# Kernel optimization log

Measured on AMD Instinct MI355X. Metric: run time of the kernel, lower is better.

Reference implementation:

```python
import jax, jax.numpy as jnp
import numpy as np

N = 50000      # input_dim == output_dim
E = 800000     # nnz in sparse weight (original: 12300 from w_ind.mat)
B = 64         # batch


def setup_inputs() -> dict:
    key = jax.random.key(0)
    k1, k2, k3, k4, k5 = jax.random.split(key, 5)
    inputs = jax.random.normal(k1, (B, N), dtype=jnp.float32)
    # truncated-normal(std=0.01) approximated by scaled normal
    W3 = 0.01 * jax.random.normal(k2, (E,), dtype=jnp.float32)
    b = jnp.zeros((N,), dtype=jnp.float32)
    # velocity = 1250 * row of CSV -> positive scale vector
    velocity = 1250.0 * jax.random.uniform(k3, (N,), dtype=jnp.float32)
    I = jax.random.randint(k4, (E,), 0, N, dtype=jnp.int64)  # row (dest) index
    J = jax.random.randint(k5, (E,), 0, N, dtype=jnp.int64)  # col (source) index
    return {"inputs": inputs, "W3": W3, "b": b, "velocity": velocity, "I": I, "J": J}


def reference(inputs, W3, b, velocity, I, J):
    # sparse W[i,j] = W3[e] scaled by velocity broadcast along rows -> * velocity[J]
    wv = W3 * velocity[J]                       # [E]
    # out = (W_sparse @ inputs^T)^T + b  == scatter-add over rows I
    contrib = inputs[:, J] * wv[None, :]        # [B, E] gather + scale
    out = jnp.zeros((inputs.shape[0], velocity.shape[0]), inputs.dtype)
    out = out.at[:, I].add(contrib)             # [B, N] scatter-add
    return out + b
```

## Files before the change

kernel.cpp:

```cpp
#include <hip/hip_runtime.h>


#define BATCH 64
#define QROWS 64
#define PCHUNK 2048
#define GCH 512
#define BCAP 32
#define BSTR 33
#define GSTR 16

typedef unsigned long long ull;

__global__ void __launch_bounds__(256) k_prep_hist(
        const float* __restrict__ in, const float* __restrict__ velocity,
        float* __restrict__ in_T,
        const int* __restrict__ I, int* __restrict__ coarse_hist,
        int NC, int N, int E, int nb_n) {
    __shared__ float tile[64 * 65];
    const int t = threadIdx.x;

    if ((int)blockIdx.x < nb_n) {
        const int n0 = blockIdx.x * 64;
        const int x  = t & 63;
        const int r  = t >> 6;
        for (int b = r; b < BATCH; b += 4) {
            float v = 0.f;
            if (n0 + x < N) v = in[(size_t)b * N + n0 + x];
            tile[x * 65 + b] = v;
        }
        __syncthreads();
        for (int xr = r; xr < 64; xr += 4) {
            if (n0 + xr < N) {
                const float vel = velocity[n0 + xr];
                in_T[(size_t)(n0 + xr) * BATCH + x] = tile[xr * 65 + x] * vel;
            }
        }
    } else {
        int* h = (int*)tile;
        for (int c = t; c < NC; c += 256) h[c] = 0;
        __syncthreads();
        const int e0 = ((int)blockIdx.x - nb_n) * PCHUNK;
        int e1 = e0 + PCHUNK; if (e1 > E) e1 = E;
        for (int e = e0 + t; e < e1; e += 256) atomicAdd(&h[I[e] >> 6], 1);
        __syncthreads();
        for (int c = t; c < NC; c += 256) if (h[c]) atomicAdd(&coarse_hist[c], h[c]);
    }
}

__global__ void __launch_bounds__(1024) k_scan(const int* __restrict__ coarse_hist,
                                               int* __restrict__ coarse_base,
                                               int* __restrict__ gcursor, int NC) {
    __shared__ int sh[1024];
    const int t = threadIdx.x;
    const int v = (t < NC) ? coarse_hist[t] : 0;
    sh[t] = v;
    __syncthreads();
    for (int off = 1; off < 1024; off <<= 1) {
        const int u = (t >= off) ? sh[t - off] : 0;
        __syncthreads();
        sh[t] += u;
        __syncthreads();
    }
    if (t < NC) { coarse_base[t] = sh[t] - v; gcursor[t * GSTR] = sh[t] - v; }
    if (t == NC - 1) coarse_base[NC] = sh[t];
}

__global__ void __launch_bounds__(512) k_partition(
        const int* __restrict__ I, const int* __restrict__ J,
        const float* __restrict__ W3,
        int* __restrict__ gcursor, ull* __restrict__ part, int E, int NC) {
    __shared__ int hist[1024];
    __shared__ int base[1024];
    const int t = threadIdx.x;
    for (int c = t; c < NC; c += 512) hist[c] = 0;
    __syncthreads();
    const int e0 = blockIdx.x * PCHUNK;
    int e1 = e0 + PCHUNK; if (e1 > E) e1 = E;

    ull  rec[4];
    int  cb[4];
    int  rk[4];
    bool ok[4];
    #pragma unroll
    for (int u = 0; u < 4; ++u) {
        const int e = e0 + u * 512 + t;
        ok[u] = (e < e1);
        cb[u] = 0; rk[u] = 0; rec[u] = 0ull;
        if (ok[u]) {
            const int i = I[e];
            const int j = J[e];
            cb[u] = i >> 6;
            rk[u] = atomicAdd(&hist[cb[u]], 1);
            rec[u] = ((ull)__float_as_uint(W3[e]) << 32)
                   | ((ull)((unsigned)(i & 63) << 16) | (unsigned)j);
        }
    }
    __syncthreads();
    for (int c = t; c < NC; c += 512) {
        const int cnt = hist[c];
        base[c] = cnt ? atomicAdd(&gcursor[c * GSTR], cnt) : 0;
    }
    __syncthreads();
    #pragma unroll
    for (int u = 0; u < 4; ++u)
        if (ok[u]) part[(size_t)base[cb[u]] + rk[u]] = rec[u];
}

__global__ void __launch_bounds__(512) k_gather(
        const float* __restrict__ in_T, const ull* __restrict__ part,
        const int* __restrict__ coarse_base, const float* __restrict__ bias,
        float* __restrict__ out, int N) {
    __shared__ ull smem[64 * BSTR + GCH];
    __shared__ int cnt[64];
    __shared__ int ocnt;
    ull* const bins = smem;
    ull* const ovf  = smem + 64 * BSTR;
    float* const tile = (float*)smem;

    const int t    = threadIdx.x;
    const int lane = t & 63;
    const int w    = t >> 6;
    const int c    = blockIdx.x;

    const int beg = coarse_base[c];
    const int end = coarse_base[c + 1];

    float acc[8];
    #pragma unroll
    for (int r = 0; r < 8; ++r) acc[r] = 0.f;

    for (int cb = beg; cb < end; cb += GCH) {
        __syncthreads();
        if (t < 64) cnt[t] = 0;
        if (t == 0) ocnt = 0;
        __syncthreads();

        const int e = cb + t;
        if (e < end) {
            const ull rec = part[e];
            const int li = (int)(((unsigned)rec >> 16) & 63u);
            const int r = atomicAdd(&cnt[li], 1);
            if (r < BCAP) bins[li * BSTR + r] = rec;
            else          ovf[atomicAdd(&ocnt, 1)] = rec;
        }
        __syncthreads();

        #pragma unroll
        for (int r8 = 0; r8 < 8; ++r8) {
            const int row = w * 8 + r8;
            int n = cnt[row]; if (n > BCAP) n = BCAP;
            const ull* bp = &bins[row * BSTR];
            float a = acc[r8];
            int k = 0;
            for (; k + 4 <= n; k += 4) {
                const ull r0 = bp[k], r1 = bp[k + 1], r2 = bp[k + 2], r3 = bp[k + 3];
                const float v0 = in_T[(int)((unsigned)r0 & 0xffffu) * BATCH + lane];
                const float v1 = in_T[(int)((unsigned)r1 & 0xffffu) * BATCH + lane];
                const float v2 = in_T[(int)((unsigned)r2 & 0xffffu) * BATCH + lane];
                const float v3 = in_T[(int)((unsigned)r3 & 0xffffu) * BATCH + lane];
                a += v0 * __uint_as_float((unsigned)(r0 >> 32));
                a += v1 * __uint_as_float((unsigned)(r1 >> 32));
                a += v2 * __uint_as_float((unsigned)(r2 >> 32));
                a += v3 * __uint_as_float((unsigned)(r3 >> 32));
            }
            for (; k < n; ++k) {
                const ull rr = bp[k];
                a += in_T[(int)((unsigned)rr & 0xffffu) * BATCH + lane]
                   * __uint_as_float((unsigned)(rr >> 32));
            }
            acc[r8] = a;
        }

        const int oc = ocnt;
        if (oc > 0) {
            #pragma unroll
            for (int r8 = 0; r8 < 8; ++r8) {
                const int row = w * 8 + r8;
                float a = acc[r8];
                for (int k = 0; k < oc; ++k) {
                    const ull rr = ovf[k];
                    if ((int)(((unsigned)rr >> 16) & 63u) == row)
                        a += in_T[(int)((unsigned)rr & 0xffffu) * BATCH + lane]
                           * __uint_as_float((unsigned)(rr >> 32));
                }
                acc[r8] = a;
            }
        }
    }

    __syncthreads();
    #pragma unroll
    for (int r8 = 0; r8 < 8; ++r8)
        tile[(w * 8 + r8) * 65 + lane] = acc[r8];
    __syncthreads();

    const int n0  = c * QROWS;
    const int row = t & 63;
    const int bq  = t >> 6;
    const int n = n0 + row;
    if (n < N) {
        const float bv = bias[n];
        for (int b = bq; b < BATCH; b += 8)
            out[(size_t)b * N + n] = tile[row * 65 + b] + bv;
    }
}

__global__ void k_edge_scatter_direct(const float* __restrict__ in,
                                      const float* __restrict__ W3,
                                      const float* __restrict__ velocity,
                                      const int* __restrict__ I,
                                      const int* __restrict__ J,
                                      float* __restrict__ out, int N, int E) {
    const int lane = threadIdx.x & 63;
    const long wave   = (long)blockIdx.x * (blockDim.x >> 6) + (threadIdx.x >> 6);
    const long nwaves = (long)gridDim.x * (blockDim.x >> 6);
    for (long base = wave * 64; base < E; base += nwaves * 64) {
        const long e = base + lane;
        int iv = 0, jv = 0; float wvv = 0.f;
        if (e < E) { iv = I[e]; jv = J[e]; wvv = W3[e] * velocity[jv]; }
        const int cnt = (int)((E - base) < 64 ? (E - base) : 64);
        for (int k = 0; k < cnt; ++k) {
            const int   ii = __shfl(iv, k);
            const int   jj = __shfl(jv, k);
            const float wvx = __shfl(wvv, k);
            const float val = in[(size_t)lane * N + jj] * wvx;
            atomicAdd(&out[(size_t)lane * N + ii], val);
        }
    }
}

__global__ void k_add_bias(const float* __restrict__ bias, float* __restrict__ out, int N, int total) {
    int idx = blockIdx.x * blockDim.x + threadIdx.x;
    if (idx < total) out[idx] += bias[idx % N];
}

extern "C" void kernel_launch(void* const* d_in, const int* in_sizes, int n_in,
                              void* d_out, int out_size, void* d_ws, size_t ws_size,
                              hipStream_t stream) {
    const float* inputs   = (const float*)d_in[0];
    const float* W3       = (const float*)d_in[1];
    const float* bias     = (const float*)d_in[2];
    const float* velocity = (const float*)d_in[3];
    const int*   I        = (const int*)d_in[4];
    const int*   J        = (const int*)d_in[5];
    const int E = in_sizes[1];
    const int N = in_sizes[3];
    float* out = (float*)d_out;

    const size_t mat_elems = (size_t)N * BATCH;
    const int NC   = (N + QROWS - 1) / QROWS;
    const int nb_n = (N + 63) / 64;
    const int nb_e = (E + PCHUNK - 1) / PCHUNK;

    const size_t need = mat_elems * sizeof(float)
                      + (size_t)E * sizeof(ull)
                      + (size_t)(NC + (NC + 1) + NC * GSTR) * sizeof(int);

    if (ws_size >= need && N <= 65535 && NC <= 1024) {
        float* in_T        = (float*)d_ws;
        ull*   part        = (ull*)(in_T + mat_elems);
        int*   coarse_hist = (int*)(part + E);
        int*   coarse_base = coarse_hist + NC;
        int*   gcursor     = coarse_base + NC + 1;

        hipMemsetAsync(coarse_hist, 0, (size_t)NC * sizeof(int), stream);
        k_prep_hist<<<nb_n + nb_e, 256,  0, stream>>>(inputs, velocity, in_T, I, coarse_hist, NC, N, E, nb_n);
        k_scan     <<<1,           1024, 0, stream>>>(coarse_hist, coarse_base, gcursor, NC);
        k_partition<<<nb_e,        512,  0, stream>>>(I, J, W3, gcursor, part, E, NC);
        k_gather   <<<NC,          512,  0, stream>>>(in_T, part, coarse_base, bias, out, N);
    } else {
        hipMemsetAsync(out, 0, (size_t)out_size * sizeof(float), stream);
        const int waves_needed   = (E + 63) / 64;
        const int scatter_blocks = (waves_needed + 3) / 4;
        k_edge_scatter_direct<<<scatter_blocks, 256, 0, stream>>>(inputs, W3, velocity, I, J, out, N, E);
        k_add_bias<<<(out_size + 255) / 256, 256, 0, stream>>>(bias, out, N, out_size);
    }
}
```

Measured before the change: 156.5 us.

## Fuse scan into prep kernel via last-block pattern and enlarge gather chunk

```diff
diff --git a/kernel.cpp b/kernel.cpp
--- a/kernel.cpp
+++ b/kernel.cpp
@@ -4,7 +4,7 @@
 #define BATCH 64
 #define QROWS 64
 #define PCHUNK 2048
-#define GCH 512
+#define GCH 1024
 #define BCAP 32
 #define BSTR 33
 #define GSTR 16
@@ -15,8 +15,12 @@
         const float* __restrict__ in, const float* __restrict__ velocity,
         float* __restrict__ in_T,
         const int* __restrict__ I, int* __restrict__ coarse_hist,
-        int NC, int N, int E, int nb_n) {
+        int* __restrict__ done, int* __restrict__ coarse_base,
+        int* __restrict__ gcursor,
+        int NC, int N, int E, int nb_n, int ntotal) {
     __shared__ float tile[64 * 65];
+    __shared__ int ps[256];
+    __shared__ int amlast;
     const int t = threadIdx.x;
 
     if ((int)blockIdx.x < nb_n) {
@@ -45,24 +49,42 @@
         __syncthreads();
         for (int c = t; c < NC; c += 256) if (h[c]) atomicAdd(&coarse_hist[c], h[c]);
     }
-}
-
-__global__ void __launch_bounds__(1024) k_scan(const int* __restrict__ coarse_hist,
-                                               int* __restrict__ coarse_base,
-                                               int* __restrict__ gcursor, int NC) {
-    __shared__ int sh[1024];
-    const int t = threadIdx.x;
-    const int v = (t < NC) ? coarse_hist[t] : 0;
-    sh[t] = v;
-    __syncthreads();
-    for (int off = 1; off < 1024; off <<= 1) {
-        const int u = (t >= off) ? sh[t - off] : 0;
-        __syncthreads();
-        sh[t] += u;
-        __syncthreads();
-    }
-    if (t < NC) { coarse_base[t] = sh[t] - v; gcursor[t * GSTR] = sh[t] - v; }
-    if (t == NC - 1) coarse_base[NC] = sh[t];
+
+    __syncthreads();
+    if (t == 0) {
+        __threadfence();
+        amlast = (atomicAdd(done, 1) == ntotal - 1) ? 1 : 0;
+    }
+    __syncthreads();
+    if (amlast) {
+        int loc[4];
+        int s = 0;
+        #pragma unroll
+        for (int k = 0; k < 4; ++k) {
+            const int c = 4 * t + k;
+            int v = 0;
+            if (c < NC) v = atomicAdd(&coarse_hist[c], 0);
+            loc[k] = s; s += v;
+        }
+        ps[t] = s;
+        __syncthreads();
+        for (int off = 1; off < 256; off <<= 1) {
+            const int u = (t >= off) ? ps[t - off] : 0;
+            __syncthreads();
+            ps[t] += u;
+            __syncthreads();
+        }
+        const int excl = ps[t] - s;
+        #pragma unroll
+        for (int k = 0; k < 4; ++k) {
+            const int c = 4 * t + k;
+            if (c < NC) {
+                coarse_base[c]    = excl + loc[k];
+                gcursor[c * GSTR] = excl + loc[k];
+            }
+        }
+        if (t == 255) coarse_base[NC] = ps[255];
+    }
 }
 
 __global__ void __launch_bounds__(512) k_partition(
@@ -135,13 +157,16 @@
         if (t == 0) ocnt = 0;
         __syncthreads();
 
-        const int e = cb + t;
-        if (e < end) {
-            const ull rec = part[e];
-            const int li = (int)(((unsigned)rec >> 16) & 63u);
-            const int r = atomicAdd(&cnt[li], 1);
-            if (r < BCAP) bins[li * BSTR + r] = rec;
-            else          ovf[atomicAdd(&ocnt, 1)] = rec;
+        #pragma unroll
+        for (int u = 0; u < 2; ++u) {
+            const int e = cb + u * 512 + t;
+            if (e < end) {
+                const ull rec = part[e];
+                const int li = (int)(((unsigned)rec >> 16) & 63u);
+                const int r = atomicAdd(&cnt[li], 1);
+                if (r < BCAP) bins[li * BSTR + r] = rec;
+                else          ovf[atomicAdd(&ocnt, 1)] = rec;
+            }
         }
         __syncthreads();
 
@@ -251,23 +276,26 @@
     const int NC   = (N + QROWS - 1) / QROWS;
     const int nb_n = (N + 63) / 64;
     const int nb_e = (E + PCHUNK - 1) / PCHUNK;
+    const int ntot = nb_n + nb_e;
 
     const size_t need = mat_elems * sizeof(float)
                       + (size_t)E * sizeof(ull)
-                      + (size_t)(NC + (NC + 1) + NC * GSTR) * sizeof(int);
+                      + (size_t)(NC + 1 + (NC + 1) + NC * GSTR) * sizeof(int);
 
     if (ws_size >= need && N <= 65535 && NC <= 1024) {
         float* in_T        = (float*)d_ws;
         ull*   part        = (ull*)(in_T + mat_elems);
         int*   coarse_hist = (int*)(part + E);
-        int*   coarse_base = coarse_hist + NC;
+        int*   done        = coarse_hist + NC;
+        int*   coarse_base = done + 1;
         int*   gcursor     = coarse_base + NC + 1;
 
-        hipMemsetAsync(coarse_hist, 0, (size_t)NC * sizeof(int), stream);
-        k_prep_hist<<<nb_n + nb_e, 256,  0, stream>>>(inputs, velocity, in_T, I, coarse_hist, NC, N, E, nb_n);
-        k_scan     <<<1,           1024, 0, stream>>>(coarse_hist, coarse_base, gcursor, NC);
-        k_partition<<<nb_e,        512,  0, stream>>>(I, J, W3, gcursor, part, E, NC);
-        k_gather   <<<NC,          512,  0, stream>>>(in_T, part, coarse_base, bias, out, N);
+        hipMemsetAsync(coarse_hist, 0, (size_t)(NC + 1) * sizeof(int), stream);
+        k_prep_hist<<<ntot, 256,  0, stream>>>(inputs, velocity, in_T, I,
+                                               coarse_hist, done, coarse_base,
+                                               gcursor, NC, N, E, nb_n, ntot);
+        k_partition<<<nb_e, 512,  0, stream>>>(I, J, W3, gcursor, part, E, NC);
+        k_gather   <<<NC,   512,  0, stream>>>(in_T, part, coarse_base, bias, out, N);
     } else {
         hipMemsetAsync(out, 0, (size_t)out_size * sizeof(float), stream);
         const int waves_needed   = (E + 63) / 64;
```

Result: slower. 176.5 us (+12.8%).
